# Performance work log

Measured on AMD Instinct MI355X. Metric: run time of the kernel, lower is better.

## Reference

```python
import jax
import jax.numpy as jnp
from jax import lax
import numpy as np

BATCH, SEQ, STATES = 64, 4096, 64


def setup_inputs() -> dict:
    key = jax.random.key(0)
    k1, k2, k3, k4 = jax.random.split(key, 4)
    scores = jax.random.normal(k1, (BATCH, SEQ, STATES), dtype=jnp.float32)
    transition = jax.random.normal(k2, (STATES, STATES), dtype=jnp.float32)
    source = jax.random.uniform(k3, (STATES,), dtype=jnp.float32)
    sink = jax.random.uniform(k4, (STATES,), dtype=jnp.float32)
    return {"scores": scores, "transition": transition, "source": source, "sink": sink}


def reference(scores, transition, source, sink):
    # Linear-chain CRF log-partition (forward algorithm in log space).
    # scores: (B, T, S) emission scores; transition: (S, S) [from, to].
    B, T, S = scores.shape
    # t == 0: original code logsumexps a broadcast-identical axis of size S,
    # which adds a constant log(S) -- reproduced here for bit-faithful math.
    score0 = source[None, :] + scores[:, 0] + jnp.log(jnp.asarray(S, scores.dtype))  # (B, S)

    def step(alpha, s_t):
        # alpha: (B, S) log-scores over previous state; s_t: (B, S) emissions at t
        new = jax.nn.logsumexp(alpha[:, :, None] + transition[None, :, :], axis=1) + s_t
        return new, None

    # scan over time: (T-1, B, S)
    alpha_final, _ = lax.scan(step, score0, jnp.swapaxes(scores[:, 1:], 0, 1))
    return jax.nn.logsumexp(alpha_final + sink[None, :], axis=1)  # (B,)
```

## Files before the change

### kernel.cpp

```cpp
#include <hip/hip_runtime.h>
#include <cstdint>


#define B_    64
#define T_    4096
#define S_    64
#define L_    9
#define NC_   455
#define WPB_  29
#define CPB_  464
#define LOG2E 1.44269504088896340736f

typedef float  f32x4  __attribute__((ext_vector_type(4)));
typedef __bf16 bf16x8 __attribute__((ext_vector_type(8)));
union U4B { uint4 u; bf16x8 b; };

__global__ __launch_bounds__(64, 2) void crf_phase1(
    const float* __restrict__ scores,
    const float* __restrict__ transition,
    float* __restrict__ Ybuf, float* __restrict__ Zbuf, float* __restrict__ Lz)
{
    __shared__ float tb[16][68];
    const int wid  = blockIdx.x;
    const bool bwd = wid >= (B_ * WPB_);
    const int wl   = bwd ? wid - B_ * WPB_ : wid;
    const int b    = wl / WPB_, wg = wl % WPB_;
    const int lane = threadIdx.x, g = lane >> 4, l = lane & 15;

    int cl = 16 * wg + l; if (cl > NC_ - 1) cl = NC_ - 1;
    const float* ap = scores + ((size_t)b * T_ + L_ * cl + (bwd ? L_ : 0)) * S_ + 8 * g;

    auto ldq = [&](int idx, f32x4* q) {
        const float* p = ap + (ptrdiff_t)idx * S_;
        q[0] = *(const f32x4*)p;        q[1] = *(const f32x4*)(p + 4);
        q[2] = *(const f32x4*)(p + 32); q[3] = *(const f32x4*)(p + 36);
    };

    f32x4 em[L_][4];
    if (!bwd) {
        #pragma unroll
        for (int r = 1; r < L_; ++r) ldq(r, em[r - 1]);
    } else {
        #pragma unroll
        for (int i = 0; i < L_; ++i) ldq(-i, em[i]);
    }

    bf16x8 BE[2][4];
    #pragma unroll
    for (int kb = 0; kb < 2; ++kb)
    #pragma unroll
    for (int nt = 0; nt < 4; ++nt) {
        bf16x8 t;
        #pragma unroll
        for (int dd = 0; dd < 4; ++dd) {
            int k0 = 32 * kb + 8 * g + 2 * dd, n = 16 * nt + l;
            float e0, e1;
            if (!bwd) { e0 = transition[k0 * 64 + n]; e1 = transition[(k0 + 1) * 64 + n]; }
            else      { e0 = transition[n * 64 + k0]; e1 = transition[n * 64 + k0 + 1]; }
            t[2 * dd]     = (__bf16)exp2f(e0 * LOG2E);
            t[2 * dd + 1] = (__bf16)exp2f(e1 * LOG2E);
        }
        BE[kb][nt] = t;
    }

    f32x4 acc[4];
    int   Lt[4] = {0, 0, 0, 0};

    auto mfma8 = [&](bf16x8 A0, bf16x8 A1) {
        #pragma unroll
        for (int nt = 0; nt < 4; ++nt) {
            f32x4 z4 = {0.f, 0.f, 0.f, 0.f};
            z4      = __builtin_amdgcn_mfma_f32_16x16x32_bf16(A0, BE[0][nt], z4, 0, 0, 0);
            acc[nt] = __builtin_amdgcn_mfma_f32_16x16x32_bf16(A1, BE[1][nt], z4, 0, 0, 0);
        }
    };
    auto renorm = [&]() {
        #pragma unroll
        for (int r = 0; r < 4; ++r) {
            float m = fmaxf(fmaxf(acc[0][r], acc[1][r]), fmaxf(acc[2][r], acc[3][r]));
            m = fmaxf(m, __shfl_xor(m, 1, 64));
            m = fmaxf(m, __shfl_xor(m, 2, 64));
            m = fmaxf(m, __shfl_xor(m, 4, 64));
            m = fmaxf(m, __shfl_xor(m, 8, 64));
            int ex = (int)(__float_as_uint(m) >> 23) - 127;
            float sc = __uint_as_float((unsigned)(127 - ex) << 23);
            Lt[r] += ex;
            #pragma unroll
            for (int nt = 0; nt < 4; ++nt) acc[nt][r] *= sc;
        }
    };
    auto xposeA = [&](const f32x4& c0, const f32x4& c1,
                      const f32x4& c2, const f32x4& c3, bf16x8& A0, bf16x8& A1) {
        #pragma unroll
        for (int nt = 0; nt < 4; ++nt)
            #pragma unroll
            for (int r = 0; r < 4; ++r)
                tb[4 * g + r][16 * nt + l] = acc[nt][r];
        __builtin_amdgcn_s_waitcnt(0xC07F);
        __builtin_amdgcn_wave_barrier();
        const float* rowp = &tb[l][8 * g];
        f32x4 x0 = *(const f32x4*)rowp;
        f32x4 x1 = *(const f32x4*)(rowp + 4);
        f32x4 x2 = *(const f32x4*)(rowp + 32);
        f32x4 x3 = *(const f32x4*)(rowp + 36);
        #pragma unroll
        for (int d = 0; d < 4; ++d) {
            A0[d]     = (__bf16)(x0[d] * exp2f(c0[d] * LOG2E));
            A0[d + 4] = (__bf16)(x1[d] * exp2f(c1[d] * LOG2E));
            A1[d]     = (__bf16)(x2[d] * exp2f(c2[d] * LOG2E));
            A1[d + 4] = (__bf16)(x3[d] * exp2f(c3[d] * LOG2E));
        }
    };

    if (!bwd) {
        { U4B t; t.u = make_uint4(0x3F803F80u, 0x3F803F80u, 0x3F803F80u, 0x3F803F80u);
          mfma8(t.b, t.b); }
        #pragma unroll
        for (int tt = 1; tt < L_; ++tt) {
            f32x4* q = em[tt - 1];
            bf16x8 A0, A1;
            xposeA(q[0], q[1], q[2], q[3], A0, A1);
            mfma8(A0, A1);
            if ((tt & 3) == 3) renorm();
        }
        float* yb = Ybuf + ((size_t)(b * WPB_ + wg) << 10);
        #pragma unroll
        for (int nt = 0; nt < 4; ++nt)
            *(f32x4*)(yb + ((nt * 64 + lane) << 2)) = acc[nt];
    } else {
        {
            f32x4* q = em[0];
            bf16x8 A0, A1;
            #pragma unroll
            for (int d = 0; d < 4; ++d) {
                A0[d]     = (__bf16)exp2f(q[0][d] * LOG2E);
                A0[d + 4] = (__bf16)exp2f(q[1][d] * LOG2E);
                A1[d]     = (__bf16)exp2f(q[2][d] * LOG2E);
                A1[d + 4] = (__bf16)exp2f(q[3][d] * LOG2E);
            }
            mfma8(A0, A1);
        }
        #pragma unroll
        for (int i = 1; i < L_; ++i) {
            f32x4* q = em[i];
            bf16x8 A0, A1;
            xposeA(q[0], q[1], q[2], q[3], A0, A1);
            mfma8(A0, A1);
            if ((i & 3) == 3) renorm();
        }
        float* zb = Zbuf + ((size_t)(b * WPB_ + wg) << 10);
        #pragma unroll
        for (int nt = 0; nt < 4; ++nt)
            *(f32x4*)(zb + ((nt * 64 + lane) << 2)) = acc[nt];
        if (l == 0) {
            #pragma unroll
            for (int r = 0; r < 4; ++r)
                Lz[b * CPB_ + 16 * wg + 4 * g + r] = (float)Lt[r];
        }
    }
}

__global__ __launch_bounds__(64) void crf_phase2(
    const float* __restrict__ scores, const float* __restrict__ source,
    const float* __restrict__ sink,
    const float* __restrict__ Ybuf, const float* __restrict__ Zbuf,
    const float* __restrict__ Lz, float* __restrict__ Pbuf)
{
    const int bw = blockIdx.x;
    const int b = bw / WPB_, wg = bw % WPB_;
    const int lane = threadIdx.x;
    const int q = lane >> 4, l = lane & 15;
    float acc = 0.f;

    const float* Yb = Ybuf + ((size_t)bw << 10);
    const float* Zb = Zbuf + ((size_t)bw << 10);
    f32x4 y[4], z[4];
    #pragma unroll
    for (int nt = 0; nt < 4; ++nt) {
        y[nt] = *(const f32x4*)(Yb + ((nt * 64 + lane) << 2));
        z[nt] = *(const f32x4*)(Zb + ((nt * 64 + lane) << 2));
    }
    float E2[4][4];
    #pragma unroll
    for (int r = 0; r < 4; ++r) {
        int c = 16 * wg + 4 * q + r; int cc = c < NC_ ? c : NC_ - 1;
        const float* er = scores + ((size_t)b * T_ + (size_t)L_ * cc + L_) * S_;
        #pragma unroll
        for (int nt = 0; nt < 4; ++nt)
            E2[r][nt] = exp2f(er[16 * nt + l] * LOG2E);
    }
    float zn3[4];
    #pragma unroll
    for (int nt = 0; nt < 4; ++nt) zn3[nt] = __shfl(z[nt][0], lane + 16, 64);
    if (q == 3 && wg + 1 < WPB_) {
        const float* Zn = Zbuf + (((size_t)bw + 1) << 10);
        #pragma unroll
        for (int nt = 0; nt < 4; ++nt) zn3[nt] = Zn[(nt * 64 + l) << 2];
    }
    float esk[4];
    #pragma unroll
    for (int nt = 0; nt < 4; ++nt) esk[nt] = exp2f(sink[16 * nt + l] * LOG2E);

    #pragma unroll
    for (int r = 0; r < 4; ++r) {
        int c = 16 * wg + 4 * q + r;
        float p = 0.f, qs = 0.f;
        #pragma unroll
        for (int nt = 0; nt < 4; ++nt) {
            float zz = (r < 3) ? z[nt][r + 1] : zn3[nt];
            if (c == NC_ - 1) zz = esk[nt];
            float ye = y[nt][r] * E2[r][nt];
            p  += ye * zz;
            qs += ye;
        }
        #pragma unroll
        for (int m = 1; m <= 8; m <<= 1) {
            p  += __shfl_xor(p, m, 64);
            qs += __shfl_xor(qs, m, 64);
        }
        if (l == 0 && c < NC_)
            acc += log2f(p) - log2f(qs) + Lz[b * CPB_ + c];
    }
    if (wg == 0 && q == 0) {
        float s0 = 0.f;
        #pragma unroll
        for (int nt = 0; nt < 4; ++nt) {
            float a0 = exp2f((source[16 * nt + l]
                              + scores[(size_t)b * T_ * S_ + 16 * nt + l]) * LOG2E);
            s0 += a0 * z[nt][0];
        }
        #pragma unroll
        for (int m = 1; m <= 8; m <<= 1) s0 += __shfl_xor(s0, m, 64);
        if (l == 0) acc += log2f(s0);
    }
    #pragma unroll
    for (int m = 32; m >= 1; m >>= 1) acc += __shfl_xor(acc, m, 64);
    if (lane == 0) Pbuf[bw] = acc;
}

__global__ __launch_bounds__(64) void crf_phase3(
    const float* __restrict__ Pbuf, float* __restrict__ out)
{
    const int b = threadIdx.x;
    float s = 0.f;
    #pragma unroll
    for (int i = 0; i < WPB_; ++i) s += Pbuf[b * WPB_ + i];
    out[b] = 0.6931471805599453f * s + 4.158883083359672f;
}

extern "C" void kernel_launch(void* const* d_in, const int* in_sizes, int n_in,
                              void* d_out, int out_size, void* d_ws, size_t ws_size,
                              hipStream_t stream) {
    (void)in_sizes; (void)n_in; (void)out_size; (void)ws_size;
    const float* scores     = (const float*)d_in[0];
    const float* transition = (const float*)d_in[1];
    const float* source     = (const float*)d_in[2];
    const float* sink       = (const float*)d_in[3];
    float* out = (float*)d_out;

    float* Ybuf = (float*)d_ws;
    float* Zbuf = Ybuf + (size_t)B_ * WPB_ * 1024;
    float* Lz   = Zbuf + (size_t)B_ * WPB_ * 1024;
    float* Pbuf = Lz   + (size_t)B_ * CPB_;

    hipLaunchKernelGGL(crf_phase1, dim3(2 * B_ * WPB_), dim3(64), 0, stream,
                       scores, transition, Ybuf, Zbuf, Lz);
    hipLaunchKernelGGL(crf_phase2, dim3(B_ * WPB_), dim3(64), 0, stream,
                       scores, source, sink, Ybuf, Zbuf, Lz, Pbuf);
    hipLaunchKernelGGL(crf_phase3, dim3(1), dim3(64), 0, stream, Pbuf, out);
}
```

Measured before the change: 131.5 us.

## Pack four waves per phase1 block and fuse phase2/phase3 into per-batch blocks

New measurement: 215.3 us. 63.7% more time.

```diff
diff --git a/kernel.cpp b/kernel.cpp
--- a/kernel.cpp
+++ b/kernel.cpp
@@ -15,17 +15,18 @@
 typedef __bf16 bf16x8 __attribute__((ext_vector_type(8)));
 union U4B { uint4 u; bf16x8 b; };
 
-__global__ __launch_bounds__(64, 2) void crf_phase1(
+__global__ __launch_bounds__(256, 8) void crf_phase1(
     const float* __restrict__ scores,
     const float* __restrict__ transition,
     float* __restrict__ Ybuf, float* __restrict__ Zbuf, float* __restrict__ Lz)
 {
-    __shared__ float tb[16][68];
-    const int wid  = blockIdx.x;
+    __shared__ float tb[4][16][68];
+    const int wv   = threadIdx.x >> 6;
+    const int wid  = blockIdx.x * 4 + wv;
     const bool bwd = wid >= (B_ * WPB_);
     const int wl   = bwd ? wid - B_ * WPB_ : wid;
     const int b    = wl / WPB_, wg = wl % WPB_;
-    const int lane = threadIdx.x, g = lane >> 4, l = lane & 15;
+    const int lane = threadIdx.x & 63, g = lane >> 4, l = lane & 15;
 
     int cl = 16 * wg + l; if (cl > NC_ - 1) cl = NC_ - 1;
     const float* ap = scores + ((size_t)b * T_ + L_ * cl + (bwd ? L_ : 0)) * S_ + 8 * g;
@@ -95,10 +96,10 @@
         for (int nt = 0; nt < 4; ++nt)
             #pragma unroll
             for (int r = 0; r < 4; ++r)
-                tb[4 * g + r][16 * nt + l] = acc[nt][r];
+                tb[wv][4 * g + r][16 * nt + l] = acc[nt][r];
         __builtin_amdgcn_s_waitcnt(0xC07F);
         __builtin_amdgcn_wave_barrier();
-        const float* rowp = &tb[l][8 * g];
+        const float* rowp = &tb[wv][l][8 * g];
         f32x4 x0 = *(const f32x4*)rowp;
         f32x4 x1 = *(const f32x4*)(rowp + 4);
         f32x4 x2 = *(const f32x4*)(rowp + 32);
@@ -160,92 +161,93 @@
     }
 }
 
-__global__ __launch_bounds__(64) void crf_phase2(
+__global__ __launch_bounds__(1024) void crf_phase2(
     const float* __restrict__ scores, const float* __restrict__ source,
     const float* __restrict__ sink,
     const float* __restrict__ Ybuf, const float* __restrict__ Zbuf,
-    const float* __restrict__ Lz, float* __restrict__ Pbuf)
+    const float* __restrict__ Lz, float* __restrict__ out)
 {
-    const int bw = blockIdx.x;
-    const int b = bw / WPB_, wg = bw % WPB_;
-    const int lane = threadIdx.x;
+    __shared__ float part[16];
+    const int b = blockIdx.x;
+    const int wv = threadIdx.x >> 6, lane = threadIdx.x & 63;
     const int q = lane >> 4, l = lane & 15;
     float acc = 0.f;
 
-    const float* Yb = Ybuf + ((size_t)bw << 10);
-    const float* Zb = Zbuf + ((size_t)bw << 10);
-    f32x4 y[4], z[4];
-    #pragma unroll
-    for (int nt = 0; nt < 4; ++nt) {
-        y[nt] = *(const f32x4*)(Yb + ((nt * 64 + lane) << 2));
-        z[nt] = *(const f32x4*)(Zb + ((nt * 64 + lane) << 2));
-    }
-    float E2[4][4];
-    #pragma unroll
-    for (int r = 0; r < 4; ++r) {
-        int c = 16 * wg + 4 * q + r; int cc = c < NC_ ? c : NC_ - 1;
-        const float* er = scores + ((size_t)b * T_ + (size_t)L_ * cc + L_) * S_;
-        #pragma unroll
-        for (int nt = 0; nt < 4; ++nt)
-            E2[r][nt] = exp2f(er[16 * nt + l] * LOG2E);
-    }
-    float zn3[4];
-    #pragma unroll
-    for (int nt = 0; nt < 4; ++nt) zn3[nt] = __shfl(z[nt][0], lane + 16, 64);
-    if (q == 3 && wg + 1 < WPB_) {
-        const float* Zn = Zbuf + (((size_t)bw + 1) << 10);
-        #pragma unroll
-        for (int nt = 0; nt < 4; ++nt) zn3[nt] = Zn[(nt * 64 + l) << 2];
-    }
     float esk[4];
     #pragma unroll
     for (int nt = 0; nt < 4; ++nt) esk[nt] = exp2f(sink[16 * nt + l] * LOG2E);
 
-    #pragma unroll
-    for (int r = 0; r < 4; ++r) {
-        int c = 16 * wg + 4 * q + r;
-        float p = 0.f, qs = 0.f;
+    for (int wg = wv; wg < WPB_; wg += 16) {
+        const int bw = b * WPB_ + wg;
+        const float* Yb = Ybuf + ((size_t)bw << 10);
+        const float* Zb = Zbuf + ((size_t)bw << 10);
+        f32x4 y[4], z[4];
         #pragma unroll
         for (int nt = 0; nt < 4; ++nt) {
-            float zz = (r < 3) ? z[nt][r + 1] : zn3[nt];
-            if (c == NC_ - 1) zz = esk[nt];
-            float ye = y[nt][r] * E2[r][nt];
-            p  += ye * zz;
-            qs += ye;
-        }
-        #pragma unroll
-        for (int m = 1; m <= 8; m <<= 1) {
-            p  += __shfl_xor(p, m, 64);
-            qs += __shfl_xor(qs, m, 64);
-        }
-        if (l == 0 && c < NC_)
-            acc += log2f(p) - log2f(qs) + Lz[b * CPB_ + c];
-    }
-    if (wg == 0 && q == 0) {
-        float s0 = 0.f;
-        #pragma unroll
-        for (int nt = 0; nt < 4; ++nt) {
-            float a0 = exp2f((source[16 * nt + l]
-                              + scores[(size_t)b * T_ * S_ + 16 * nt + l]) * LOG2E);
-            s0 += a0 * z[nt][0];
-        }
-        #pragma unroll
-        for (int m = 1; m <= 8; m <<= 1) s0 += __shfl_xor(s0, m, 64);
-        if (l == 0) acc += log2f(s0);
+            y[nt] = *(const f32x4*)(Yb + ((nt * 64 + lane) << 2));
+            z[nt] = *(const f32x4*)(Zb + ((nt * 64 + lane) << 2));
+        }
+        float E2[4][4];
+        #pragma unroll
+        for (int r = 0; r < 4; ++r) {
+            int c = 16 * wg + 4 * q + r; int cc = c < NC_ ? c : NC_ - 1;
+            const float* er = scores + ((size_t)b * T_ + (size_t)L_ * cc + L_) * S_;
+            #pragma unroll
+            for (int nt = 0; nt < 4; ++nt)
+                E2[r][nt] = exp2f(er[16 * nt + l] * LOG2E);
+        }
+        float zn3[4];
+        #pragma unroll
+        for (int nt = 0; nt < 4; ++nt) zn3[nt] = __shfl(z[nt][0], lane + 16, 64);
+        if (q == 3 && wg + 1 < WPB_) {
+            const float* Zn = Zbuf + (((size_t)bw + 1) << 10);
+            #pragma unroll
+            for (int nt = 0; nt < 4; ++nt) zn3[nt] = Zn[(nt * 64 + l) << 2];
+        }
+
+        #pragma unroll
+        for (int r = 0; r < 4; ++r) {
+            int c = 16 * wg + 4 * q + r;
+            float p = 0.f, qs = 0.f;
+            #pragma unroll
+            for (int nt = 0; nt < 4; ++nt) {
+                float zz = (r < 3) ? z[nt][r + 1] : zn3[nt];
+                if (c == NC_ - 1) zz = esk[nt];
+                float ye = y[nt][r] * E2[r][nt];
+                p  += ye * zz;
+                qs += ye;
+            }
+            #pragma unroll
+            for (int m = 1; m <= 8; m <<= 1) {
+                p  += __shfl_xor(p, m, 64);
+                qs += __shfl_xor(qs, m, 64);
+            }
+            if (l == 0 && c < NC_)
+                acc += log2f(p) - log2f(qs) + Lz[b * CPB_ + c];
+        }
+        if (wg == 0 && q == 0) {
+            float s0 = 0.f;
+            #pragma unroll
+            for (int nt = 0; nt < 4; ++nt) {
+                float a0 = exp2f((source[16 * nt + l]
+                                  + scores[(size_t)b * T_ * S_ + 16 * nt + l]) * LOG2E);
+                s0 += a0 * z[nt][0];
+            }
+            #pragma unroll
+            for (int m = 1; m <= 8; m <<= 1) s0 += __shfl_xor(s0, m, 64);
+            if (l == 0) acc += log2f(s0);
+        }
     }
     #pragma unroll
     for (int m = 32; m >= 1; m >>= 1) acc += __shfl_xor(acc, m, 64);
-    if (lane == 0) Pbuf[bw] = acc;
-}
-
-__global__ __launch_bounds__(64) void crf_phase3(
-    const float* __restrict__ Pbuf, float* __restrict__ out)
-{
-    const int b = threadIdx.x;
-    float s = 0.f;
-    #pragma unroll
-    for (int i = 0; i < WPB_; ++i) s += Pbuf[b * WPB_ + i];
-    out[b] = 0.6931471805599453f * s + 4.158883083359672f;
+    if (lane == 0) part[wv] = acc;
+    __syncthreads();
+    if (threadIdx.x == 0) {
+        float s = 0.f;
+        #pragma unroll
+        for (int i = 0; i < 16; ++i) s += part[i];
+        out[b] = 0.6931471805599453f * s + 4.158883083359672f;
+    }
 }
 
 extern "C" void kernel_launch(void* const* d_in, const int* in_sizes, int n_in,
@@ -261,11 +263,9 @@
     float* Ybuf = (float*)d_ws;
     float* Zbuf = Ybuf + (size_t)B_ * WPB_ * 1024;
     float* Lz   = Zbuf + (size_t)B_ * WPB_ * 1024;
-    float* Pbuf = Lz   + (size_t)B_ * CPB_;
-
-    hipLaunchKernelGGL(crf_phase1, dim3(2 * B_ * WPB_), dim3(64), 0, stream,
+
+    hipLaunchKernelGGL(crf_phase1, dim3(2 * B_ * WPB_ / 4), dim3(256), 0, stream,
                        scores, transition, Ybuf, Zbuf, Lz);
-    hipLaunchKernelGGL(crf_phase2, dim3(B_ * WPB_), dim3(64), 0, stream,
-                       scores, source, sink, Ybuf, Zbuf, Lz, Pbuf);
-    hipLaunchKernelGGL(crf_phase3, dim3(1), dim3(64), 0, stream, Pbuf, out);
+    hipLaunchKernelGGL(crf_phase2, dim3(B_), dim3(1024), 0, stream,
+                       scores, source, sink, Ybuf, Zbuf, Lz, out);
 }
```
